# Kernel optimization log

Measured on AMD Instinct MI355X. Metric: run time of the kernel, lower is better.

Reference implementation:

```python
import jax, jax.numpy as jnp
import numpy as np

B, T, D, H, J = 64, 128, 768, 256, 128  # batch, tokens, input_dim, span_hidden_dim, top_injection_dim
PRUNING_RATIO = 2.0


def setup_inputs() -> dict:
    key = jax.random.key(0)
    ks = jax.random.split(key, 12)
    def w(k, shape, fan_in):
        return jax.random.normal(k, shape, jnp.float32) / np.sqrt(fan_in)
    return {
        "inputs": jax.random.normal(ks[0], (B, T, D), jnp.float32),
        "input_mask": jnp.ones((B, T), jnp.int32),
        "top_injection_embedding": jax.random.normal(ks[1], (B, J), jnp.float32),
        # SpanRepAssembly: start / end projections
        "W_start": w(ks[2], (D, H), D), "b_start": jnp.zeros((H,), jnp.float32),
        "W_end": w(ks[3], (D, H), D), "b_end": jnp.zeros((H,), jnp.float32),
        # span_scorer: ReLU -> Linear(H,H) -> ReLU -> Linear(H,1)
        "W_s1": w(ks[4], (H, H), H), "b_s1": jnp.zeros((H,), jnp.float32),
        "W_s2": w(ks[5], (H, 1), H), "b_s2": jnp.zeros((1,), jnp.float32),
        # top injection path
        "W_inj": w(ks[6], (J, H), J), "b_inj": jnp.zeros((H,), jnp.float32),
        "W_sec": w(ks[7], (H, H), H), "b_sec": jnp.zeros((H,), jnp.float32),
        "W_pred": w(ks[8], (H, 1), H), "b_pred": jnp.zeros((1,), jnp.float32),
    }


def reference(inputs, input_mask, top_injection_embedding,
              W_start, b_start, W_end, b_end,
              W_s1, b_s1, W_s2, b_s2,
              W_inj, b_inj, W_sec, b_sec, W_pred, b_pred):
    b, t, _ = inputs.shape
    k_spans = int(PRUNING_RATIO * t)
    # SpanRepAssembly: span_hidden[b, (s,e)] = startProj(x_s) + endProj(x_e), s <= e,
    # flattened start-major (matches start_end_range ordering).
    A = inputs @ W_start + b_start                      # [B,T,H]
    E = inputs @ W_end + b_end                          # [B,T,H]
    s_idx, e_idx = jnp.triu_indices(t)                  # N = T(T+1)/2 spans, row-major
    span_hidden = A[:, s_idx] + E[:, e_idx]             # [B,N,H]
    m = input_mask.astype(jnp.float32)
    span_mask = m[:, s_idx] * m[:, e_idx]               # [B,N]
    # span_scorer MLP over all spans
    h = jax.nn.relu(span_hidden) @ W_s1 + b_s1
    scores = (jax.nn.relu(h) @ W_s2 + b_s2)[..., 0]     # [B,N]
    # SpanPruner: mask invalid spans to -inf, top-k, sort indices, gather
    masked_scores = jnp.where(span_mask > 0, scores, -jnp.inf)
    _, top_idx = jax.lax.top_k(masked_scores, k_spans)  # [B,K]
    top_idx = jnp.sort(top_idx, axis=1)
    top_span_hidden = jnp.take_along_axis(span_hidden, top_idx[:, :, None], axis=1)  # [B,K,H]
    top_span_mask = jnp.take_along_axis(span_mask, top_idx, axis=1)[..., None]       # [B,K,1]
    top_span_scores = jnp.take_along_axis(masked_scores, top_idx, axis=1)[..., None] # [B,K,1]
    top_span_scores = jnp.where(jnp.isinf(top_span_scores), -1.0, top_span_scores)
    # top-injection scoring head
    inj = (top_injection_embedding @ W_inj + b_inj)[:, None, :]      # [B,1,H]
    sec = top_span_hidden @ W_sec + b_sec                            # [B,K,H]
    top_span_logits = jax.nn.relu(inj + sec) @ W_pred + b_pred + top_span_scores  # [B,K,1]
    top_span_probs = jax.nn.sigmoid(top_span_logits) * top_span_mask
    return top_span_probs
```

## Files before the change

kernel.cpp:

```cpp
#include <hip/hip_runtime.h>
#include <hip/hip_bf16.h>
#include <math.h>

#define BB 64
#define T 128
#define DD 768
#define H 256
#define JJ 128
#define NSPAN 8256
#define KTOP 256
#define SCAP 1024
#define MARGIN 0.03f

typedef __attribute__((ext_vector_type(8))) short bf16x8;
typedef __attribute__((ext_vector_type(4))) float f32x4;

__device__ inline unsigned short bfrne(float x) {
    unsigned u = __float_as_uint(x);
    return (unsigned short)((u + 0x7FFFu + ((u >> 16) & 1u)) >> 16);
}

__device__ inline unsigned pk2(float x, float y) {
    float2 f; f.x = x; f.y = y;
    __hip_bfloat162 h = __float22bfloat162_rn(f);
    return *reinterpret_cast<unsigned*>(&h);
}

template<int CTRL>
__device__ __forceinline__ float dpp_add16(float v) {
    return v + __int_as_float(__builtin_amdgcn_update_dpp(
        0, __float_as_int(v), CTRL, 0xF, 0xF, true));
}

__global__ __launch_bounds__(256) void prep_proj_kernel(
    const float* __restrict__ X,
    const float* __restrict__ Wa, const float* __restrict__ ba,
    const float* __restrict__ Wb, const float* __restrict__ bb,
    float* __restrict__ AE,
    int* __restrict__ s_idx, int* __restrict__ e_idx,
    const float* __restrict__ W1, unsigned short* __restrict__ Wpk,
    const float* __restrict__ tie, const float* __restrict__ Winj,
    const float* __restrict__ binj, float* __restrict__ injv)
{
    const int blk = blockIdx.x;
    const int t = threadIdx.x;

    if (blk >= 512) {
        const int pblk = blk - 512;
        if (pblk == 0) {
            if (t < T) {
                int s = t;
                int start = s * T - (s * (s - 1)) / 2;
                int len = T - s;
                for (int i = 0; i < len; ++i) {
                    s_idx[start + i] = s;
                    e_idx[start + i] = s + i;
                }
            }
        } else if (pblk <= 256) {
            int idx = (pblk - 1) * 256 + t;
            int j  = idx & 7;
            int l  = (idx >> 3) & 63;
            int kc = (idx >> 9) & 7;
            int ct = idx >> 12;
            int k = kc * 32 + (l >> 4) * 8 + j;
            int n = ct * 16 + (l & 15);
            Wpk[idx] = bfrne(W1[k * 256 + n]);
        } else {
            int b = pblk - 257;
            __shared__ float tb[JJ];
            if (t < JJ) tb[t] = tie[b * JJ + t];
            __syncthreads();
            float a = binj[t];
            for (int j = 0; j < JJ; ++j)
                a = fmaf(tb[j], Winj[j * H + t], a);
            injv[b * H + t] = a;
        }
        return;
    }

    const int px = blk & 127;
    const int cb = blk >> 7;
    const int m0 = px * 64;
    const float* W    = (cb < 2) ? Wa : Wb;
    const float* bias = (cb < 2) ? ba : bb;
    const int wc0 = (cb & 1) * 128;
    const int oc0 = (cb < 2) ? wc0 : (256 + wc0);

    __shared__ __align__(16) float Xs[32 * 68];
    __shared__ __align__(16) float Wl[32 * 140];

    const int tx = t & 15;
    const int ty = t >> 4;

    const int xrow = t >> 2;
    const int xk8  = (t & 3) * 8;
    const int wrow = t >> 4;
    const int wi   = t & 15;
    const int wro  = wi * 8 + ((wi >> 2) << 2);

    float4 xr[2], w0r[2], w1r[2];
    {
        const float* xp = &X[(size_t)(m0 + xrow) * DD + xk8];
        xr[0] = *(const float4*)&xp[0]; xr[1] = *(const float4*)&xp[4];
        const float* wp0 = &W[(size_t)wrow * 256 + wc0 + wi * 8];
        w0r[0] = *(const float4*)&wp0[0]; w0r[1] = *(const float4*)&wp0[4];
        const float* wp1 = &W[(size_t)(wrow + 16) * 256 + wc0 + wi * 8];
        w1r[0] = *(const float4*)&wp1[0]; w1r[1] = *(const float4*)&wp1[4];
    }

    float acc[4][8];
#pragma unroll
    for (int i = 0; i < 4; ++i)
#pragma unroll
        for (int j = 0; j < 8; ++j) acc[i][j] = 0.f;

    for (int it = 0; it < 24; ++it) {
        __syncthreads();
        Xs[(xk8 + 0) * 68 + xrow] = xr[0].x;
        Xs[(xk8 + 1) * 68 + xrow] = xr[0].y;
        Xs[(xk8 + 2) * 68 + xrow] = xr[0].z;
        Xs[(xk8 + 3) * 68 + xrow] = xr[0].w;
        Xs[(xk8 + 4) * 68 + xrow] = xr[1].x;
        Xs[(xk8 + 5) * 68 + xrow] = xr[1].y;
        Xs[(xk8 + 6) * 68 + xrow] = xr[1].z;
        Xs[(xk8 + 7) * 68 + xrow] = xr[1].w;
        *(float4*)&Wl[wrow * 140 + wro]          = w0r[0];
        *(float4*)&Wl[wrow * 140 + wro + 4]      = w0r[1];
        *(float4*)&Wl[(wrow + 16) * 140 + wro]   = w1r[0];
        *(float4*)&Wl[(wrow + 16) * 140 + wro + 4] = w1r[1];
        __syncthreads();
        if (it + 1 < 24) {
            const int kk = (it + 1) * 32;
            const float* xp = &X[(size_t)(m0 + xrow) * DD + kk + xk8];
            xr[0] = *(const float4*)&xp[0]; xr[1] = *(const float4*)&xp[4];
            const float* wp0 = &W[(size_t)(kk + wrow) * 256 + wc0 + wi * 8];
            w0r[0] = *(const float4*)&wp0[0]; w0r[1] = *(const float4*)&wp0[4];
            const float* wp1 = &W[(size_t)(kk + wrow + 16) * 256 + wc0 + wi * 8];
            w1r[0] = *(const float4*)&wp1[0]; w1r[1] = *(const float4*)&wp1[4];
        }
#pragma unroll
        for (int k = 0; k < 32; ++k) {
            float4 wv0 = *(const float4*)&Wl[k * 140 + wro];
            float4 wv1 = *(const float4*)&Wl[k * 140 + wro + 4];
            float wq[8] = {wv0.x, wv0.y, wv0.z, wv0.w, wv1.x, wv1.y, wv1.z, wv1.w};
            float4 xv = *(const float4*)&Xs[k * 68 + ty * 4];
            float xq[4] = {xv.x, xv.y, xv.z, xv.w};
#pragma unroll
            for (int i = 0; i < 4; ++i)
#pragma unroll
                for (int j = 0; j < 8; ++j)
                    acc[i][j] = fmaf(xq[i], wq[j], acc[i][j]);
        }
    }

    float bq[8];
#pragma unroll
    for (int j = 0; j < 8; ++j) bq[j] = bias[wc0 + tx * 8 + j];
#pragma unroll
    for (int i = 0; i < 4; ++i) {
        const size_t row = m0 + ty * 4 + i;
        float4 o0, o1;
        o0.x = acc[i][0] + bq[0]; o0.y = acc[i][1] + bq[1];
        o0.z = acc[i][2] + bq[2]; o0.w = acc[i][3] + bq[3];
        o1.x = acc[i][4] + bq[4]; o1.y = acc[i][5] + bq[5];
        o1.z = acc[i][6] + bq[6]; o1.w = acc[i][7] + bq[7];
        *(float4*)&AE[row * 512 + oc0 + tx * 8]     = o0;
        *(float4*)&AE[row * 512 + oc0 + tx * 8 + 4] = o1;
    }
}

__global__ __launch_bounds__(512, 4) void approx_kernel(
    const float* __restrict__ AE,
    const unsigned short* __restrict__ Wpk,
    const float* __restrict__ bs1, const float* __restrict__ Ws2,
    const float* __restrict__ bs2g,
    const int* __restrict__ s_idx, const int* __restrict__ e_idx,
    const int* __restrict__ maskp,
    float* __restrict__ scores)
{
    const int bid   = blockIdx.x;
    const int r     = bid & 7;
    const int q     = bid >> 3;
    const int g     = q >> 3;
    const int chunk = q & 7;
    const int b     = g * 8 + r;
    const int tile0 = chunk * 65;
    const int tcnt  = (516 - tile0 < 65) ? (516 - tile0) : 65;

    __shared__ __align__(16) unsigned short rshf[2][8][64][8];
    __shared__ float pslice[2][8][16];

    const int t      = threadIdx.x;
    const int w      = t >> 6;
    const int lane   = t & 63;
    const int lrow16 = lane & 15;
    const int quad   = lane >> 4;

    bf16x8 bfr[2][8];
    float b1c[2], w2c[2];
#pragma unroll
    for (int c = 0; c < 2; ++c) {
#pragma unroll
        for (int kc = 0; kc < 8; ++kc)
            bfr[c][kc] = *(const bf16x8*)&Wpk[((((2 * w + c) * 8 + kc) * 64) + lane) * 8];
        int col = (2 * w + c) * 16 + lrow16;
        b1c[c] = bs1[col];
        w2c[c] = Ws2[col];
    }
    const float bs2v = bs2g[0];

    const float* Abase = AE + (size_t)b * T * 512;
    const int sp   = t >> 5;
    const int km   = t & 31;
    const int kc_s = km >> 2;
    const int q_s  = km & 3;
    const int slot = (q_s * 16 + sp + kc_s) & 63;

    {
        int n = tile0 * 16 + sp;
        int s = s_idx[n], e = e_idx[n];
        const float* Ar = Abase + (size_t)s * 512 + km * 8;
        const float* Er = Abase + (size_t)e * 512 + 256 + km * 8;
        float4 a0 = *(const float4*)&Ar[0];
        float4 a1 = *(const float4*)&Ar[4];
        float4 e0 = *(const float4*)&Er[0];
        float4 e1 = *(const float4*)&Er[4];
        uint4 v;
        v.x = pk2(fmaxf(a0.x + e0.x, 0.f), fmaxf(a0.y + e0.y, 0.f));
        v.y = pk2(fmaxf(a0.z + e0.z, 0.f), fmaxf(a0.w + e0.w, 0.f));
        v.z = pk2(fmaxf(a1.x + e1.x, 0.f), fmaxf(a1.y + e1.y, 0.f));
        v.w = pk2(fmaxf(a1.z + e1.z, 0.f), fmaxf(a1.w + e1.w, 0.f));
        *(uint4*)&rshf[0][kc_s][slot][0] = v;
    }
    int s_nx = 0, e_nx = 0;
    if (tcnt > 1) {
        int n = (tile0 + 1) * 16 + sp;
        s_nx = s_idx[n]; e_nx = e_idx[n];
    }
    __syncthreads();

    for (int tt = 0; tt < tcnt; ++tt) {
        const int cur = tt & 1;
        float4 a0, a1, e0, e1;
        const bool pf = (tt + 1 < tcnt);
        if (pf) {
            const float* Ar = Abase + (size_t)s_nx * 512 + km * 8;
            const float* Er = Abase + (size_t)e_nx * 512 + 256 + km * 8;
            a0 = *(const float4*)&Ar[0];
            a1 = *(const float4*)&Ar[4];
            e0 = *(const float4*)&Er[0];
            e1 = *(const float4*)&Er[4];
        }
        if (tt + 2 < tcnt) {
            int n = (tile0 + tt + 2) * 16 + sp;
            s_nx = s_idx[n]; e_nx = e_idx[n];
        }
        f32x4 acc0 = {0.f, 0.f, 0.f, 0.f};
        f32x4 acc1 = {0.f, 0.f, 0.f, 0.f};
#pragma unroll
        for (int kc = 0; kc < 8; ++kc) {
            bf16x8 a = *(const bf16x8*)&rshf[cur][kc][(lane + kc) & 63][0];
            acc0 = __builtin_amdgcn_mfma_f32_16x16x32_bf16(a, bfr[0][kc], acc0, 0, 0, 0);
            acc1 = __builtin_amdgcn_mfma_f32_16x16x32_bf16(a, bfr[1][kc], acc1, 0, 0, 0);
        }
        float ps[4];
#pragma unroll
        for (int rr = 0; rr < 4; ++rr)
            ps[rr] = fmaxf(acc0[rr] + b1c[0], 0.f) * w2c[0]
                   + fmaxf(acc1[rr] + b1c[1], 0.f) * w2c[1];
#pragma unroll
        for (int rr = 0; rr < 4; ++rr) {
            float v = ps[rr];
            v = dpp_add16<0xB1>(v);
            v = dpp_add16<0x4E>(v);
            v = dpp_add16<0x141>(v);
            v = dpp_add16<0x140>(v);
            ps[rr] = v;
        }
        if (lrow16 == 0) {
            float4 v; v.x = ps[0]; v.y = ps[1]; v.z = ps[2]; v.w = ps[3];
            *(float4*)&pslice[cur][w][quad * 4] = v;
        }
        if (pf) {
            uint4 v;
            v.x = pk2(fmaxf(a0.x + e0.x, 0.f), fmaxf(a0.y + e0.y, 0.f));
            v.y = pk2(fmaxf(a0.z + e0.z, 0.f), fmaxf(a0.w + e0.w, 0.f));
            v.z = pk2(fmaxf(a1.x + e1.x, 0.f), fmaxf(a1.y + e1.y, 0.f));
            v.w = pk2(fmaxf(a1.z + e1.z, 0.f), fmaxf(a1.w + e1.w, 0.f));
            *(uint4*)&rshf[cur ^ 1][kc_s][slot][0] = v;
        }
        __syncthreads();
        if (t < 16) {
            int n = (tile0 + tt) * 16 + t;
            float sc = bs2v;
#pragma unroll
            for (int ww = 0; ww < 8; ++ww) sc += pslice[cur][ww][t];
            int s = s_idx[n], e = e_idx[n];
            bool m = (maskp[b * T + s] != 0) && (maskp[b * T + e] != 0);
            scores[(size_t)b * NSPAN + n] = m ? sc : -INFINITY;
        }
    }
}

__global__ __launch_bounds__(1024) void select_kernel(
    const float* __restrict__ scores,
    int* __restrict__ shortlist, int* __restrict__ slcnt)
{
    const int b = blockIdx.x;
    const int t = threadIdx.x;
    __shared__ unsigned su[NSPAN];
    __shared__ int hist[256];
    __shared__ unsigned s_prefix;
    __shared__ int s_remaining;
    __shared__ int wave_keep[16];

    const float* sc = scores + (size_t)b * NSPAN;
    for (int i = t; i < NSPAN; i += 1024) {
        unsigned ub = __float_as_uint(sc[i]);
        su[i] = (ub & 0x80000000u) ? ~ub : (ub | 0x80000000u);
    }
    __syncthreads();

    unsigned prefix = 0;
    int remaining = KTOP;
    for (int d = 3; d >= 0; --d) {
        if (t < 256) hist[t] = 0;
        __syncthreads();
        const int sh = d * 8;
        for (int i = t; i < NSPAN; i += 1024) {
            unsigned u = su[i];
            bool match = (d == 3) || ((u >> (sh + 8)) == (prefix >> (sh + 8)));
            if (match) atomicAdd(&hist[(u >> sh) & 255], 1);
        }
        __syncthreads();
        if (t == 0) {
            int acc = 0, v = 255;
            for (; v > 0; --v) {
                int h = hist[v];
                if (acc + h >= remaining) break;
                acc += h;
            }
            s_prefix = prefix | ((unsigned)v << sh);
            s_remaining = remaining - acc;
        }
        __syncthreads();
        prefix = s_prefix;
        remaining = s_remaining;
        __syncthreads();
    }

    unsigned ub = (prefix & 0x80000000u) ? (prefix & 0x7FFFFFFFu) : ~prefix;
    float kthf = __uint_as_float(ub);
    float tau = kthf - MARGIN;
    unsigned tb = __float_as_uint(tau);
    unsigned ktau = (tb & 0x80000000u) ? ~tb : (tb | 0x80000000u);

    const int wid = t >> 6, lane = t & 63;
    int base = 0;
    const unsigned long long ltmask = (1ull << lane) - 1ull;
    for (int c0 = 0; c0 < NSPAN; c0 += 1024) {
        int n = c0 + t;
        bool keep = (n < NSPAN) && (su[n] >= ktau);
        unsigned long long bk = __ballot(keep);
        int before = __popcll(bk & ltmask);
        if (lane == 0) wave_keep[wid] = __popcll(bk);
        __syncthreads();
        int kb = base;
        for (int wv = 0; wv < wid; ++wv) kb += wave_keep[wv];
        if (keep) {
            int pos = kb + before;
            if (pos < SCAP) shortlist[b * SCAP + pos] = n;
        }
        for (int wv = 0; wv < 16; ++wv) base += wave_keep[wv];
        __syncthreads();
    }
    if (t == 0) slcnt[b] = base < SCAP ? base : SCAP;
}

__global__ __launch_bounds__(512) void exact_kernel(
    const float* __restrict__ AE,
    const float* __restrict__ Ws1, const float* __restrict__ bs1,
    const float* __restrict__ Ws2, const float* __restrict__ bs2g,
    const int* __restrict__ s_idx, const int* __restrict__ e_idx,
    const int* __restrict__ shortlist, const int* __restrict__ slcnt,
    float* __restrict__ scores)
{
    const int b  = blockIdx.y;
    const int n0 = blockIdx.x * 64;
    const int cntb = slcnt[b];
    if (n0 >= cntb) return;

    __shared__ float rsh[64][36];
    __shared__ float Ws[32][260];
    __shared__ int   ss[64], se[64], nn[64];

    const int t = threadIdx.x;
    if (t < 64) {
        int row = n0 + t;
        int n = 0;
        if (row < cntb) n = shortlist[b * SCAP + row];
        nn[t] = (row < cntb) ? n : -1;
        ss[t] = s_idx[n]; se[t] = e_idx[n];
    }
    __syncthreads();

    const int tx = t & 31;
    const int ty = t >> 5;
    float acc[4][8];
#pragma unroll
    for (int i = 0; i < 4; ++i)
#pragma unroll
        for (int j = 0; j < 8; ++j) acc[i][j] = 0.f;

    const float* Abase = AE + (size_t)b * T * 512;

    for (int kk = 0; kk < 256; kk += 32) {
        __syncthreads();
        {
            int row = t >> 4, q4 = (t & 15) * 4;
#pragma unroll
            for (int q = 0; q < 4; ++q)
                *(float4*)&Ws[row][q4 + q * 64] =
                    *(const float4*)&Ws1[(size_t)(kk + row) * 256 + q4 + q * 64];
        }
        {
            int sp = t >> 3, k4 = (t & 7) * 4;
            const float* Ar = Abase + (size_t)ss[sp] * 512 + kk + k4;
            const float* Er = Abase + (size_t)se[sp] * 512 + 256 + kk + k4;
            float4 a = *(const float4*)Ar;
            float4 e = *(const float4*)Er;
            float4 v;
            v.x = fmaxf(a.x + e.x, 0.f); v.y = fmaxf(a.y + e.y, 0.f);
            v.z = fmaxf(a.z + e.z, 0.f); v.w = fmaxf(a.w + e.w, 0.f);
            *(float4*)&rsh[sp][k4] = v;
        }
        __syncthreads();
#pragma unroll
        for (int k4 = 0; k4 < 32; k4 += 4) {
            float w[4][8];
#pragma unroll
            for (int kq = 0; kq < 4; ++kq) {
                float4 w0 = *(const float4*)&Ws[k4 + kq][tx * 4];
                float4 w1 = *(const float4*)&Ws[k4 + kq][128 + tx * 4];
                w[kq][0] = w0.x; w[kq][1] = w0.y; w[kq][2] = w0.z; w[kq][3] = w0.w;
                w[kq][4] = w1.x; w[kq][5] = w1.y; w[kq][6] = w1.z; w[kq][7] = w1.w;
            }
#pragma unroll
            for (int i = 0; i < 4; ++i) {
                float4 rv = *(const float4*)&rsh[ty * 4 + i][k4];
                float rq[4] = {rv.x, rv.y, rv.z, rv.w};
#pragma unroll
                for (int kq = 0; kq < 4; ++kq)
#pragma unroll
                    for (int j = 0; j < 8; ++j)
                        acc[i][j] = fmaf(rq[kq], w[kq][j], acc[i][j]);
            }
        }
    }

    float b1[8], w2[8];
#pragma unroll
    for (int j = 0; j < 8; ++j) {
        int c = (j < 4) ? (tx * 4 + j) : (128 + tx * 4 + j - 4);
        b1[j] = bs1[c];
        w2[j] = Ws2[c];
    }
    const float bs2v = bs2g[0];
#pragma unroll
    for (int i = 0; i < 4; ++i) {
        int r = ty * 4 + i;
        float p = 0.f;
#pragma unroll
        for (int j = 0; j < 8; ++j)
            p += fmaxf(acc[i][j] + b1[j], 0.f) * w2[j];
#pragma unroll
        for (int off = 16; off > 0; off >>= 1)
            p += __shfl_down(p, off, 32);
        if (tx == 0) {
            int n = nn[r];
            if (n >= 0)
                scores[(size_t)b * NSPAN + n] = p + bs2v;
        }
    }
}

__global__ __launch_bounds__(1024) void topk_kernel(
    const float* __restrict__ scores,
    const int* __restrict__ shortlist, const int* __restrict__ slcnt,
    int* __restrict__ top_idx, float* __restrict__ top_scores)
{
    const int b = blockIdx.x;
    const int t = threadIdx.x;
    const int cnt = slcnt[b];

    __shared__ unsigned su[SCAP];
    __shared__ int sn[SCAP];
    __shared__ int hist[256];
    __shared__ unsigned s_prefix;
    __shared__ int s_remaining;
    __shared__ int wave_eq[16], wave_keep[16];

    for (int i = t; i < cnt; i += 1024) {
        int n = shortlist[b * SCAP + i];
        unsigned ub = __float_as_uint(scores[(size_t)b * NSPAN + n]);
        su[i] = (ub & 0x80000000u) ? ~ub : (ub | 0x80000000u);
        sn[i] = n;
    }
    __syncthreads();

    unsigned prefix = 0;
    int remaining = KTOP;
    for (int d = 3; d >= 0; --d) {
        if (t < 256) hist[t] = 0;
        __syncthreads();
        const int sh = d * 8;
        for (int i = t; i < cnt; i += 1024) {
            unsigned u = su[i];
            bool match = (d == 3) || ((u >> (sh + 8)) == (prefix >> (sh + 8)));
            if (match) atomicAdd(&hist[(u >> sh) & 255], 1);
        }
        __syncthreads();
        if (t == 0) {
            int acc = 0, v = 255;
            for (; v > 0; --v) {
                int h = hist[v];
                if (acc + h >= remaining) break;
                acc += h;
            }
            s_prefix = prefix | ((unsigned)v << sh);
            s_remaining = remaining - acc;
        }
        __syncthreads();
        prefix = s_prefix;
        remaining = s_remaining;
        __syncthreads();
    }
    const unsigned v = prefix;
    const int need_eq = remaining;

    const int wid = t >> 6, lane = t & 63;
    int base_eq = 0, base_keep = 0;
    const unsigned long long ltmask = (1ull << lane) - 1ull;
    for (int c0 = 0; c0 < cnt; c0 += 1024) {
        int i = c0 + t;
        bool valid = i < cnt;
        unsigned u = valid ? su[i] : 0u;
        bool eq = valid && (u == v);
        bool gt = valid && (u > v);
        unsigned long long beq = __ballot(eq);
        int eq_before = __popcll(beq & ltmask);
        if (lane == 0) wave_eq[wid] = __popcll(beq);
        __syncthreads();
        int eqb = base_eq;
        for (int w = 0; w < wid; ++w) eqb += wave_eq[w];
        int eq_rank = eqb + eq_before;
        bool keep = gt || (eq && (eq_rank < need_eq));
        unsigned long long bk = __ballot(keep);
        int keep_before = __popcll(bk & ltmask);
        if (lane == 0) wave_keep[wid] = __popcll(bk);
        __syncthreads();
        int kb = base_keep;
        for (int w = 0; w < wid; ++w) kb += wave_keep[w];
        if (keep) {
            int pos = kb + keep_before;
            top_idx[b * KTOP + pos] = sn[i];
            unsigned fb = (u & 0x80000000u) ? (u & 0x7FFFFFFFu) : ~u;
            float f = __uint_as_float(fb);
            top_scores[b * KTOP + pos] = isinf(f) ? -1.0f : f;
        }
        for (int w = 0; w < 16; ++w) { base_eq += wave_eq[w]; base_keep += wave_keep[w]; }
        __syncthreads();
    }
}

__global__ __launch_bounds__(256) void final_kernel(
    const float* __restrict__ AE,
    const int* __restrict__ s_idx, const int* __restrict__ e_idx,
    const int* __restrict__ maskp,
    const int* __restrict__ top_idx, const float* __restrict__ top_scores,
    const float* __restrict__ injv,
    const float* __restrict__ Wsec, const float* __restrict__ bsec,
    const float* __restrict__ Wpred, const float* __restrict__ bpredg,
    float* __restrict__ out)
{
    const int b = blockIdx.x >> 2;
    const int k0 = (blockIdx.x & 3) * 64;

    __shared__ float sh[64][36];
    __shared__ float Ws[32][260];
    __shared__ int ss[64], se[64];
    __shared__ float msk[64], tsc[64];

    const int t = threadIdx.x;
    if (t < 64) {
        int kidx = k0 + t;
        int n = top_idx[b * KTOP + kidx];
        int s = s_idx[n], e = e_idx[n];
        ss[t] = s; se[t] = e;
        msk[t] = (maskp[b * T + s] != 0 && maskp[b * T + e] != 0) ? 1.f : 0.f;
        tsc[t] = top_scores[b * KTOP + kidx];
    }
    __syncthreads();

    const int tx = t & 31;
    const int ty = t >> 5;
    float acc[8][8];
#pragma unroll
    for (int i = 0; i < 8; ++i)
#pragma unroll
        for (int j = 0; j < 8; ++j) acc[i][j] = 0.f;

    const float* Abase = AE + (size_t)b * T * 512;

    for (int kk = 0; kk < 256; kk += 32) {
        __syncthreads();
        {
            int c4 = (t & 63) * 4, r0 = t >> 6;
#pragma unroll
            for (int r8 = 0; r8 < 8; ++r8) {
                int row = r0 + r8 * 4;
                *(float4*)&Ws[row][c4] =
                    *(const float4*)&Wsec[(size_t)(kk + row) * 256 + c4];
            }
        }
        {
            int sp = t >> 2, k8 = (t & 3) * 8;
            const float* Ar = Abase + (size_t)ss[sp] * 512 + kk + k8;
            const float* Er = Abase + (size_t)se[sp] * 512 + 256 + kk + k8;
#pragma unroll
            for (int q = 0; q < 2; ++q) {
                float4 a = *(const float4*)&Ar[q * 4];
                float4 e = *(const float4*)&Er[q * 4];
                float4 v;
                v.x = a.x + e.x; v.y = a.y + e.y; v.z = a.z + e.z; v.w = a.w + e.w;
                *(float4*)&sh[sp][k8 + q * 4] = v;
            }
        }
        __syncthreads();
#pragma unroll
        for (int k4 = 0; k4 < 32; k4 += 4) {
            float w[4][8];
#pragma unroll
            for (int kq = 0; kq < 4; ++kq) {
                float4 w0 = *(const float4*)&Ws[k4 + kq][tx * 4];
                float4 w1 = *(const float4*)&Ws[k4 + kq][128 + tx * 4];
                w[kq][0] = w0.x; w[kq][1] = w0.y; w[kq][2] = w0.z; w[kq][3] = w0.w;
                w[kq][4] = w1.x; w[kq][5] = w1.y; w[kq][6] = w1.z; w[kq][7] = w1.w;
            }
#pragma unroll
            for (int i = 0; i < 8; ++i) {
                float4 rv = *(const float4*)&sh[ty * 8 + i][k4];
                float rq[4] = {rv.x, rv.y, rv.z, rv.w};
#pragma unroll
                for (int kq = 0; kq < 4; ++kq)
#pragma unroll
                    for (int j = 0; j < 8; ++j)
                        acc[i][j] = fmaf(rq[kq], w[kq][j], acc[i][j]);
            }
        }
    }

    float bsec_r[8], wpred_r[8], injr[8];
#pragma unroll
    for (int j = 0; j < 8; ++j) {
        int c = (j < 4) ? (tx * 4 + j) : (128 + tx * 4 + j - 4);
        bsec_r[j] = bsec[c];
        wpred_r[j] = Wpred[c];
        injr[j] = injv[b * H + c];
    }
    const float bp = bpredg[0];
#pragma unroll
    for (int i = 0; i < 8; ++i) {
        int r = ty * 8 + i;
        float p = 0.f;
#pragma unroll
        for (int j = 0; j < 8; ++j) {
            float sec = acc[i][j] + bsec_r[j];
            p += fmaxf(injr[j] + sec, 0.f) * wpred_r[j];
        }
#pragma unroll
        for (int off = 16; off > 0; off >>= 1)
            p += __shfl_down(p, off, 32);
        if (tx == 0) {
            float logit = p + bp + tsc[r];
            float prob = (1.f / (1.f + expf(-logit))) * msk[r];
            out[b * KTOP + k0 + r] = prob;
        }
    }
}

extern "C" void kernel_launch(void* const* d_in, const int* in_sizes, int n_in,
                              void* d_out, int out_size, void* d_ws, size_t ws_size,
                              hipStream_t stream) {
    const float* inputs  = (const float*)d_in[0];
    const int*   imask   = (const int*)d_in[1];
    const float* tie     = (const float*)d_in[2];
    const float* W_start = (const float*)d_in[3];
    const float* b_start = (const float*)d_in[4];
    const float* W_end   = (const float*)d_in[5];
    const float* b_end   = (const float*)d_in[6];
    const float* W_s1    = (const float*)d_in[7];
    const float* b_s1    = (const float*)d_in[8];
    const float* W_s2    = (const float*)d_in[9];
    const float* b_s2    = (const float*)d_in[10];
    const float* W_inj   = (const float*)d_in[11];
    const float* b_inj   = (const float*)d_in[12];
    const float* W_sec   = (const float*)d_in[13];
    const float* b_sec   = (const float*)d_in[14];
    const float* W_pred  = (const float*)d_in[15];
    const float* b_pred  = (const float*)d_in[16];
    float* out = (float*)d_out;

    float* AE         = (float*)d_ws;
    float* scores     = AE + (size_t)BB * T * 512;
    int*   s_idx      = (int*)(scores + (size_t)BB * NSPAN);
    int*   e_idx      = s_idx + NSPAN;
    int*   top_idx    = e_idx + NSPAN;
    float* top_scores = (float*)(top_idx + BB * KTOP);
    float* injv       = top_scores + BB * KTOP;
    unsigned short* Wpk = (unsigned short*)(injv + BB * H);
    int*   shortlist  = (int*)(Wpk + 65536);
    int*   slcnt      = shortlist + BB * SCAP;

    prep_proj_kernel<<<833, 256, 0, stream>>>(inputs, W_start, b_start, W_end, b_end, AE,
                                              s_idx, e_idx, W_s1, Wpk,
                                              tie, W_inj, b_inj, injv);
    approx_kernel<<<512, 512, 0, stream>>>(AE, Wpk, b_s1, W_s2, b_s2,
                                           s_idx, e_idx, imask, scores);
    select_kernel<<<BB, 1024, 0, stream>>>(scores, shortlist, slcnt);
    exact_kernel<<<dim3(16, BB), 512, 0, stream>>>(AE, W_s1, b_s1, W_s2, b_s2,
                                                   s_idx, e_idx, shortlist, slcnt, scores);
    topk_kernel<<<BB, 1024, 0, stream>>>(scores, shortlist, slcnt, top_idx, top_scores);
    final_kernel<<<BB * 4, 256, 0, stream>>>(AE, s_idx, e_idx, imask, top_idx, top_scores,
                                             injv, W_sec, b_sec, W_pred, b_pred, out);
}
```

Baseline: 482.6 us.

## Enlarge projection GEMM tile to 128 rows with swizzled row-major X staging

The fp32 start/end projection GEMM now uses 128-row tiles instead of 64, so each thread computes an 8x8 output block and the grid drops from 512 to 256 projection blocks. X is staged in shared memory row-major with an XOR swizzle and float4 stores, replacing the scalar transposed writes. The aim is more FMAs per shared-memory load and cheaper LDS staging. The cost is more registers per thread and fewer blocks to fill the GPU.

```diff
diff --git a/kernel.cpp b/kernel.cpp
--- a/kernel.cpp
+++ b/kernel.cpp
@@ -45,8 +45,8 @@
     const int blk = blockIdx.x;
     const int t = threadIdx.x;
 
-    if (blk >= 512) {
-        const int pblk = blk - 512;
+    if (blk >= 256) {
+        const int pblk = blk - 256;
         if (pblk == 0) {
             if (t < T) {
                 int s = t;
@@ -79,78 +79,90 @@
         return;
     }
 
-    const int px = blk & 127;
-    const int cb = blk >> 7;
-    const int m0 = px * 64;
+    const int px = blk & 63;
+    const int cb = blk >> 6;
+    const int m0 = px * 128;
     const float* W    = (cb < 2) ? Wa : Wb;
     const float* bias = (cb < 2) ? ba : bb;
     const int wc0 = (cb & 1) * 128;
     const int oc0 = (cb < 2) ? wc0 : (256 + wc0);
 
-    __shared__ __align__(16) float Xs[32 * 68];
+    __shared__ __align__(16) float Xs[128 * 36];
     __shared__ __align__(16) float Wl[32 * 140];
 
     const int tx = t & 15;
     const int ty = t >> 4;
-
-    const int xrow = t >> 2;
-    const int xk8  = (t & 3) * 8;
+    const int ty7 = ty & 7;
+    const int wro = tx * 8 + ((tx >> 2) << 2);
+
+    const int xrow = t >> 1;
+    const int xh   = t & 1;
+    const int xsw  = (xrow >> 3) & 7;
     const int wrow = t >> 4;
     const int wi   = t & 15;
-    const int wro  = wi * 8 + ((wi >> 2) << 2);
-
-    float4 xr[2], w0r[2], w1r[2];
+
+    float4 xg[4], w0r[2], w1r[2];
     {
-        const float* xp = &X[(size_t)(m0 + xrow) * DD + xk8];
-        xr[0] = *(const float4*)&xp[0]; xr[1] = *(const float4*)&xp[4];
+        const float* xp = &X[(size_t)(m0 + xrow) * DD];
+#pragma unroll
+        for (int q = 0; q < 4; ++q)
+            xg[q] = *(const float4*)&xp[(2 * q + xh) * 4];
         const float* wp0 = &W[(size_t)wrow * 256 + wc0 + wi * 8];
         w0r[0] = *(const float4*)&wp0[0]; w0r[1] = *(const float4*)&wp0[4];
         const float* wp1 = &W[(size_t)(wrow + 16) * 256 + wc0 + wi * 8];
         w1r[0] = *(const float4*)&wp1[0]; w1r[1] = *(const float4*)&wp1[4];
     }
 
-    float acc[4][8];
-#pragma unroll
-    for (int i = 0; i < 4; ++i)
+    float acc[8][8];
+#pragma unroll
+    for (int i = 0; i < 8; ++i)
 #pragma unroll
         for (int j = 0; j < 8; ++j) acc[i][j] = 0.f;
 
     for (int it = 0; it < 24; ++it) {
         __syncthreads();
-        Xs[(xk8 + 0) * 68 + xrow] = xr[0].x;
-        Xs[(xk8 + 1) * 68 + xrow] = xr[0].y;
-        Xs[(xk8 + 2) * 68 + xrow] = xr[0].z;
-        Xs[(xk8 + 3) * 68 + xrow] = xr[0].w;
-        Xs[(xk8 + 4) * 68 + xrow] = xr[1].x;
-        Xs[(xk8 + 5) * 68 + xrow] = xr[1].y;
-        Xs[(xk8 + 6) * 68 + xrow] = xr[1].z;
-        Xs[(xk8 + 7) * 68 + xrow] = xr[1].w;
-        *(float4*)&Wl[wrow * 140 + wro]          = w0r[0];
-        *(float4*)&Wl[wrow * 140 + wro + 4]      = w0r[1];
-        *(float4*)&Wl[(wrow + 16) * 140 + wro]   = w1r[0];
+#pragma unroll
+        for (int q = 0; q < 4; ++q) {
+            const int kb = 2 * q + xh;
+            *(float4*)&Xs[xrow * 36 + ((kb ^ xsw) << 2)] = xg[q];
+        }
+        *(float4*)&Wl[wrow * 140 + wro]            = w0r[0];
+        *(float4*)&Wl[wrow * 140 + wro + 4]        = w0r[1];
+        *(float4*)&Wl[(wrow + 16) * 140 + wro]     = w1r[0];
         *(float4*)&Wl[(wrow + 16) * 140 + wro + 4] = w1r[1];
         __syncthreads();
         if (it + 1 < 24) {
             const int kk = (it + 1) * 32;
-            const float* xp = &X[(size_t)(m0 + xrow) * DD + kk + xk8];
-            xr[0] = *(const float4*)&xp[0]; xr[1] = *(const float4*)&xp[4];
+            const float* xp = &X[(size_t)(m0 + xrow) * DD + kk];
+#pragma unroll
+            for (int q = 0; q < 4; ++q)
+                xg[q] = *(const float4*)&xp[(2 * q + xh) * 4];
             const float* wp0 = &W[(size_t)(kk + wrow) * 256 + wc0 + wi * 8];
             w0r[0] = *(const float4*)&wp0[0]; w0r[1] = *(const float4*)&wp0[4];
             const float* wp1 = &W[(size_t)(kk + wrow + 16) * 256 + wc0 + wi * 8];
             w1r[0] = *(const float4*)&wp1[0]; w1r[1] = *(const float4*)&wp1[4];
         }
 #pragma unroll
-        for (int k = 0; k < 32; ++k) {
-            float4 wv0 = *(const float4*)&Wl[k * 140 + wro];
-            float4 wv1 = *(const float4*)&Wl[k * 140 + wro + 4];
-            float wq[8] = {wv0.x, wv0.y, wv0.z, wv0.w, wv1.x, wv1.y, wv1.z, wv1.w};
-            float4 xv = *(const float4*)&Xs[k * 68 + ty * 4];
-            float xq[4] = {xv.x, xv.y, xv.z, xv.w};
-#pragma unroll
-            for (int i = 0; i < 4; ++i)
-#pragma unroll
-                for (int j = 0; j < 8; ++j)
-                    acc[i][j] = fmaf(xq[i], wq[j], acc[i][j]);
+        for (int kb = 0; kb < 8; ++kb) {
+            float4 xv[8];
+#pragma unroll
+            for (int r8 = 0; r8 < 8; ++r8)
+                xv[r8] = *(const float4*)&Xs[(ty * 8 + r8) * 36 + ((kb ^ ty7) << 2)];
+#pragma unroll
+            for (int j = 0; j < 4; ++j) {
+                const int k = kb * 4 + j;
+                float4 wv0 = *(const float4*)&Wl[k * 140 + wro];
+                float4 wv1 = *(const float4*)&Wl[k * 140 + wro + 4];
+                float wq[8] = {wv0.x, wv0.y, wv0.z, wv0.w, wv1.x, wv1.y, wv1.z, wv1.w};
+#pragma unroll
+                for (int r8 = 0; r8 < 8; ++r8) {
+                    const float xv1 = j == 0 ? xv[r8].x : j == 1 ? xv[r8].y
+                                    : j == 2 ? xv[r8].z : xv[r8].w;
+#pragma unroll
+                    for (int c = 0; c < 8; ++c)
+                        acc[r8][c] = fmaf(xv1, wq[c], acc[r8][c]);
+                }
+            }
         }
     }
 
@@ -158,13 +170,13 @@
 #pragma unroll
     for (int j = 0; j < 8; ++j) bq[j] = bias[wc0 + tx * 8 + j];
 #pragma unroll
-    for (int i = 0; i < 4; ++i) {
-        const size_t row = m0 + ty * 4 + i;
+    for (int r8 = 0; r8 < 8; ++r8) {
+        const size_t row = m0 + ty * 8 + r8;
         float4 o0, o1;
-        o0.x = acc[i][0] + bq[0]; o0.y = acc[i][1] + bq[1];
-        o0.z = acc[i][2] + bq[2]; o0.w = acc[i][3] + bq[3];
-        o1.x = acc[i][4] + bq[4]; o1.y = acc[i][5] + bq[5];
-        o1.z = acc[i][6] + bq[6]; o1.w = acc[i][7] + bq[7];
+        o0.x = acc[r8][0] + bq[0]; o0.y = acc[r8][1] + bq[1];
+        o0.z = acc[r8][2] + bq[2]; o0.w = acc[r8][3] + bq[3];
+        o1.x = acc[r8][4] + bq[4]; o1.y = acc[r8][5] + bq[5];
+        o1.z = acc[r8][6] + bq[6]; o1.w = acc[r8][7] + bq[7];
         *(float4*)&AE[row * 512 + oc0 + tx * 8]     = o0;
         *(float4*)&AE[row * 512 + oc0 + tx * 8 + 4] = o1;
     }
@@ -723,7 +735,7 @@
     int*   shortlist  = (int*)(Wpk + 65536);
     int*   slcnt      = shortlist + BB * SCAP;
 
-    prep_proj_kernel<<<833, 256, 0, stream>>>(inputs, W_start, b_start, W_end, b_end, AE,
+    prep_proj_kernel<<<577, 256, 0, stream>>>(inputs, W_start, b_start, W_end, b_end, AE,
                                               s_idx, e_idx, W_s1, Wpk,
                                               tie, W_inj, b_inj, injv);
     approx_kernel<<<512, 512, 0, stream>>>(AE, Wpk, b_s1, W_s2, b_s2,
```

Result: slower. 500.5 us (+3.7%).
